# Kernel tuning notes

Measured on AMD Instinct MI355X. Metric: run time of the kernel, lower is better.

Reference implementation:

```python
import jax, jax.numpy as jnp
import numpy as np

V, NSEG, MAXLEN, D, H = 32000, 2, 512, 768, 12
HS = D // H  # head_size = 64
B, T, NMASK = 16, 512, 20
LN_EPS = 1e-5


def setup_inputs() -> dict:
    key = jax.random.key(0)
    ks = jax.random.split(key, 16)
    s = 0.02
    return {
        "sequence": jax.random.randint(ks[0], (B, T), 0, V),
        "segment": jax.random.randint(ks[1], (B, T), 0, NSEG),
        "attn_mask": jax.random.randint(ks[2], (B, T), 0, 2).astype(jnp.int32),
        "masked_pos": jax.random.randint(ks[3], (B, NMASK), 0, T),
        "tok_emb": jax.random.normal(ks[4], (V, D), jnp.float32) * s,
        "seg_emb": jax.random.normal(ks[5], (NSEG, D), jnp.float32) * s,
        "pos_emb": jax.random.normal(ks[6], (MAXLEN, D), jnp.float32) * s,
        "ln_g": jnp.ones((D,), jnp.float32),
        "ln_b": jnp.zeros((D,), jnp.float32),
        "Wq": jax.random.normal(ks[7], (H, D, HS), jnp.float32) * s,
        "Wk": jax.random.normal(ks[8], (H, D, HS), jnp.float32) * s,
        "Wv": jax.random.normal(ks[9], (H, D, HS), jnp.float32) * s,
        "W_lm": jax.random.normal(ks[10], (D, V), jnp.float32) * s,
        "b_lm": jnp.zeros((V,), jnp.float32),
        "W_cls": jax.random.normal(ks[11], (D, 2), jnp.float32) * s,
        "b_cls": jnp.zeros((2,), jnp.float32),
    }


def reference(sequence, segment, attn_mask, masked_pos,
              tok_emb, seg_emb, pos_emb, ln_g, ln_b,
              Wq, Wk, Wv, W_lm, b_lm, W_cls, b_cls):
    Tlen = sequence.shape[1]
    # --- BERTEmbedding (dropout = identity in eval) ---
    emb = tok_emb[sequence] + seg_emb[segment] + pos_emb[jnp.arange(Tlen)][None]  # [B,T,D]
    mu = jnp.mean(emb, axis=-1, keepdims=True)
    var = jnp.mean(jnp.square(emb - mu), axis=-1, keepdims=True)
    x = (emb - mu) * jax.lax.rsqrt(var + LN_EPS) * ln_g + ln_b  # [B,T,D]

    # --- Multi-head attention (heads batched instead of Python loop) ---
    q = jnp.einsum('btd,hds->bhts', x, Wq)
    k = jnp.einsum('btd,hds->bhts', x, Wk)
    v = jnp.einsum('btd,hds->bhts', x, Wv)
    wei = jnp.einsum('bhts,bhus->bhtu', q, k) * (HS ** -0.5)  # [B,H,T,T]
    # original: wei.masked_fill(attn_mask[:, :, None] == 0, -1e-11) -> masks over query dim
    wei = jnp.where(attn_mask[:, None, :, None] == 0, jnp.float32(-1e-11), wei)
    wei = jax.nn.softmax(wei, axis=-1)
    out = jnp.einsum('bhtu,bhus->bhts', wei, v)  # [B,H,T,HS]
    x = out.transpose(0, 2, 1, 3).reshape(out.shape[0], Tlen, H * HS)  # cat heads -> [B,T,D]

    # --- Output heads ---
    x_masked = jnp.take_along_axis(x, masked_pos[:, :, None], axis=1)  # [B,NMASK,D]
    logits_lm = x_masked @ W_lm + b_lm          # [B,NMASK,V]
    logits_clsf = x[:, 0, :] @ W_cls + b_cls    # [B,2]
    return (logits_lm, logits_clsf)
```

## Files before the change

### kernel.cpp

```cpp
#include <hip/hip_runtime.h>
#include <hip/hip_bf16.h>

#define V_     32000
#define NSEG_  2
#define MAXLEN_ 512
#define D_     768
#define H_     12
#define HS_    64
#define B_     16
#define T_     512
#define NMASK_ 20
#define LN_EPS_ 1e-5f

typedef __hip_bfloat16 bf16;
typedef unsigned short ushortT;
typedef __attribute__((ext_vector_type(8))) short short8;
typedef __attribute__((ext_vector_type(4))) float f32x4;
typedef __attribute__((ext_vector_type(4))) unsigned int u32x4;

__device__ __forceinline__ ushortT f2bu(float f) {
    bf16 h = __float2bfloat16(f);
    return *reinterpret_cast<ushortT*>(&h);
}

__global__ void k_embed_ln(const int* __restrict__ seq, const int* __restrict__ seg,
                           const float* __restrict__ tok, const float* __restrict__ sege,
                           const float* __restrict__ pos, const float* __restrict__ g,
                           const float* __restrict__ bb, ushortT* __restrict__ xb) {
    int row = blockIdx.x;
    int t = row % T_;
    int tid = threadIdx.x;
    __shared__ float sbuf[D_];
    __shared__ float wsum[4], wsq[4];

    int sidx = seq[row];
    int gidx = seg[row];

    float lsum = 0.f, lsq = 0.f;
    for (int j = tid; j < D_; j += 256) {
        float e = tok[(size_t)sidx * D_ + j] + sege[(size_t)gidx * D_ + j] + pos[(size_t)t * D_ + j];
        sbuf[j] = e;
        lsum += e;
        lsq  += e * e;
    }
    #pragma unroll
    for (int o = 32; o > 0; o >>= 1) {
        lsum += __shfl_down(lsum, o);
        lsq  += __shfl_down(lsq, o);
    }
    if ((tid & 63) == 0) { wsum[tid >> 6] = lsum; wsq[tid >> 6] = lsq; }
    __syncthreads();
    float s  = wsum[0] + wsum[1] + wsum[2] + wsum[3];
    float sq = wsq[0] + wsq[1] + wsq[2] + wsq[3];
    float mean = s * (1.0f / D_);
    float var  = sq * (1.0f / D_) - mean * mean;
    float rstd = rsqrtf(var + LN_EPS_);
    for (int j = tid; j < D_; j += 256) {
        xb[(size_t)row * D_ + j] = f2bu((sbuf[j] - mean) * rstd * g[j] + bb[j]);
    }
}

__global__ void k_prep_wqkv(const float* __restrict__ Wq, const float* __restrict__ Wk,
                            const float* __restrict__ Wv, ushortT* __restrict__ Wt) {
    int blk = blockIdx.x;
    int which = blk / H_, h = blk % H_;
    int kc = blockIdx.y * 64;
    const float* W = (which == 0) ? Wq : (which == 1) ? Wk : Wv;
    __shared__ float tile[64][65];
    int tid = threadIdx.x, c = tid & 63, rgrp = tid >> 6;
    for (int kk = rgrp; kk < 64; kk += 4)
        tile[kk][c] = W[((size_t)h * D_ + kc + kk) * HS_ + c];
    __syncthreads();
    for (int ss = rgrp; ss < 64; ss += 4)
        Wt[((size_t)which * D_ + h * HS_ + ss) * D_ + kc + c] = f2bu(tile[c][ss]);
}

__global__ void k_transpose_lm(const float* __restrict__ W, ushortT* __restrict__ Wt) {
    __shared__ float tile[64][65];
    int v0 = blockIdx.x * 64, d0 = blockIdx.y * 64;
    int tid = threadIdx.x, c = tid & 63;
    for (int rr = tid >> 6; rr < 64; rr += 4)
        tile[rr][c] = W[(size_t)(d0 + rr) * V_ + v0 + c];
    __syncthreads();
    for (int rr = tid >> 6; rr < 64; rr += 4)
        Wt[(size_t)(v0 + rr) * D_ + d0 + c] = f2bu(tile[c][rr]);
}

__global__ void k_gather_xm(const float* __restrict__ x2, const int* __restrict__ masked_pos,
                            ushortT* __restrict__ xm) {
    int r = blockIdx.x;
    int tid = threadIdx.x;
    if (r < B_ * NMASK_) {
        int b = r / NMASK_, m = r % NMASK_;
        int t = masked_pos[b * NMASK_ + m];
        for (int d = tid; d < D_; d += 256)
            xm[(size_t)r * D_ + d] = f2bu(x2[((size_t)b * T_ + t) * D_ + d]);
    } else {
        for (int d = tid; d < D_; d += 256)
            xm[(size_t)r * D_ + d] = 0;
    }
}

__device__ __forceinline__ void stage_tile(const ushortT* __restrict__ A,
                                           const ushortT* __restrict__ Bt,
                                           int m0, int n0, int k0,
                                           ushortT* As, ushortT* Bs,
                                           int w, int lane) {
    #pragma unroll
    for (int i = 0; i < 2; ++i) {
        int slot = w * 64 + lane + i * 256;
        int row = slot >> 2, col = (slot & 3) * 8;
        __builtin_amdgcn_global_load_lds(
            (const __attribute__((address_space(1))) void*)(A + (size_t)(m0 + row) * D_ + k0 + col),
            (__attribute__((address_space(3))) void*)(As + (w * 64 + i * 256) * 8),
            16, 0, 0);
        __builtin_amdgcn_global_load_lds(
            (const __attribute__((address_space(1))) void*)(Bt + (size_t)(n0 + row) * D_ + k0 + col),
            (__attribute__((address_space(3))) void*)(Bs + (w * 64 + i * 256) * 8),
            16, 0, 0);
    }
}

__device__ __forceinline__ void gemm128_2ph(const ushortT* __restrict__ A,
                                            const ushortT* __restrict__ Bt,
                                            int m0, int n0,
                                            ushortT* lds,
                                            f32x4 acc[4][4]) {
    const int NT = D_ / 32;
    int tid = threadIdx.x;
    int lane = tid & 63, w = tid >> 6;
    int wr = (w >> 1) * 64, wc = (w & 1) * 64;
    int l16 = lane & 15, lk = lane >> 4;

    #pragma unroll
    for (int i = 0; i < 4; ++i)
        #pragma unroll
        for (int j = 0; j < 4; ++j)
            acc[i][j] = (f32x4){0.f, 0.f, 0.f, 0.f};

    stage_tile(A, Bt, m0, n0, 0, lds, lds + 4096, w, lane);
    asm volatile("s_waitcnt vmcnt(0)" ::: "memory");
    __builtin_amdgcn_s_barrier();

    for (int t = 0; t < NT; ++t) {
        int cur = (t & 1) * 8192;
        int nxt = 8192 - cur;
        if (t + 1 < NT)
            stage_tile(A, Bt, m0, n0, (t + 1) * 32, lds + nxt, lds + nxt + 4096, w, lane);

        const ushortT* Asc = lds + cur;
        const ushortT* Bsc = lds + cur + 4096;
        short8 a[4], bfr[4];
        #pragma unroll
        for (int i = 0; i < 4; ++i) {
            a[i]   = *(const short8*)(Asc + (wr + i * 16 + l16) * 32 + lk * 8);
            bfr[i] = *(const short8*)(Bsc + (wc + i * 16 + l16) * 32 + lk * 8);
        }
        #pragma unroll
        for (int i = 0; i < 4; ++i)
            #pragma unroll
            for (int j = 0; j < 4; ++j)
                acc[i][j] = __builtin_amdgcn_mfma_f32_16x16x32_bf16(a[i], bfr[j], acc[i][j], 0, 0, 0);

        asm volatile("s_waitcnt vmcnt(0)" ::: "memory");
        __builtin_amdgcn_s_barrier();
    }
}

__global__ __launch_bounds__(256, 4)
void k_gemm_qkv(const ushortT* __restrict__ xb, const ushortT* __restrict__ WcatT,
                ushortT* __restrict__ qb, ushortT* __restrict__ kb,
                ushortT* __restrict__ vb) {
    __shared__ ushortT lds[16384];
    f32x4 acc[4][4];
    int lin = (blockIdx.x & 7) * 144 + (blockIdx.x >> 3);
    int n0 = (lin % 18) * 128, m0 = (lin / 18) * 128;
    gemm128_2ph(xb, WcatT, m0, n0, lds, acc);

    int lane = threadIdx.x & 63, w = threadIdx.x >> 6;
    int wr = (w >> 1) * 64, wc = (w & 1) * 64;
    int l16 = lane & 15, lk = lane >> 4;
    #pragma unroll
    for (int j = 0; j < 4; ++j) {
        int n = n0 + wc + j * 16 + l16;
        int which = n / D_;
        int rem = n - which * D_;
        int h = rem >> 6, s = rem & 63;
        ushortT* outp = (which == 0) ? qb : (which == 1) ? kb : vb;
        #pragma unroll
        for (int i = 0; i < 4; ++i) {
            #pragma unroll
            for (int r = 0; r < 4; ++r) {
                int m = m0 + wr + i * 16 + lk * 4 + r;
                int b = m >> 9, t = m & (T_ - 1);
                outp[((size_t)(b * H_ + h) * T_ + t) * HS_ + s] = f2bu(acc[i][j][r]);
            }
        }
    }
}

__global__ __launch_bounds__(256, 4)
void k_gemm_lm(const ushortT* __restrict__ xm, const ushortT* __restrict__ WlmT,
               const float* __restrict__ blm, float* __restrict__ out) {
    __shared__ ushortT lds[16384];
    f32x4 acc[4][4];
    int m0 = blockIdx.x * 128, n0 = blockIdx.y * 128;
    gemm128_2ph(xm, WlmT, m0, n0, lds, acc);

    int lane = threadIdx.x & 63, w = threadIdx.x >> 6;
    int wr = (w >> 1) * 64, wc = (w & 1) * 64;
    int l16 = lane & 15, lk = lane >> 4;
    #pragma unroll
    for (int j = 0; j < 4; ++j) {
        int n = n0 + wc + j * 16 + l16;
        float bias = blm[n];
        #pragma unroll
        for (int i = 0; i < 4; ++i) {
            #pragma unroll
            for (int r = 0; r < 4; ++r) {
                int m = m0 + wr + i * 16 + lk * 4 + r;
                if (m < B_ * NMASK_)
                    out[(size_t)m * V_ + n] = acc[i][j][r] + bias;
            }
        }
    }
}

__global__ __launch_bounds__(256, 4)
void k_attn_mfma(const ushortT* __restrict__ qb, const ushortT* __restrict__ kb,
                 const ushortT* __restrict__ vb, const int* __restrict__ attn_mask,
                 float* __restrict__ x2) {
    int lin = (blockIdx.x & 7) * 192 + (blockIdx.x >> 3);
    int qt = lin & 7, bh = lin >> 3;
    int b = bh / H_, h = bh % H_;
    int tid = threadIdx.x, lane = tid & 63, w = tid >> 6;
    int l16 = lane & 15, lk = lane >> 4;

    __shared__ ushortT QP[64][72];
    __shared__ ushortT Ks[64][72];
    __shared__ ushortT Vts[64][72];
    __shared__ float mskS[64];

    const ushortT* Qg = qb + ((size_t)bh * T_ + qt * 64) * HS_;
    #pragma unroll
    for (int i = 0; i < 2; ++i) {
        int slot = tid + i * 256;
        int r = slot >> 3, c8 = (slot & 7) * 8;
        *(u32x4*)(&QP[r][c8]) = *(const u32x4*)(Qg + (size_t)r * HS_ + c8);
    }
    if (tid < 64)
        mskS[tid] = attn_mask[b * T_ + qt * 64 + tid] ? 0.125f : 0.0f;
    __syncthreads();

    short8 aq[2];
    #pragma unroll
    for (int ks = 0; ks < 2; ++ks)
        aq[ks] = *(const short8*)(&QP[w * 16 + l16][ks * 32 + lk * 8]);
    float mrow[4];
    #pragma unroll
    for (int r = 0; r < 4; ++r)
        mrow[r] = mskS[w * 16 + lk * 4 + r];

    float lsum[4];
    f32x4 accO[4];
    #pragma unroll
    for (int r = 0; r < 4; ++r) lsum[r] = 0.f;
    #pragma unroll
    for (int j = 0; j < 4; ++j)
        accO[j] = (f32x4){0.f, 0.f, 0.f, 0.f};

    for (int kt = 0; kt < 8; ++kt) {
        __syncthreads();
        {
            int r = tid >> 2, c = (tid & 3) * 16;
            const ushortT* Kg = kb + ((size_t)bh * T_ + kt * 64 + r) * HS_ + c;
            *(u32x4*)(&Ks[r][c])     = *(const u32x4*)(Kg);
            *(u32x4*)(&Ks[r][c + 8]) = *(const u32x4*)(Kg + 8);
        }
        {
            int r = lane;
            int c = w * 16;
            const ushortT* Vg = vb + ((size_t)bh * T_ + kt * 64 + r) * HS_ + c;
            short8 v0 = *(const short8*)(Vg);
            short8 v1 = *(const short8*)(Vg + 8);
            #pragma unroll
            for (int e = 0; e < 8; ++e) Vts[c + e][r]     = (ushortT)v0[e];
            #pragma unroll
            for (int e = 0; e < 8; ++e) Vts[c + 8 + e][r] = (ushortT)v1[e];
        }
        __syncthreads();

        f32x4 accS[4];
        #pragma unroll
        for (int j = 0; j < 4; ++j)
            accS[j] = (f32x4){0.f, 0.f, 0.f, 0.f};
        #pragma unroll
        for (int ks = 0; ks < 2; ++ks) {
            short8 bk[4];
            #pragma unroll
            for (int j = 0; j < 4; ++j)
                bk[j] = *(const short8*)(&Ks[j * 16 + l16][ks * 32 + lk * 8]);
            #pragma unroll
            for (int j = 0; j < 4; ++j)
                accS[j] = __builtin_amdgcn_mfma_f32_16x16x32_bf16(aq[ks], bk[j], accS[j], 0, 0, 0);
        }

        #pragma unroll
        for (int r = 0; r < 4; ++r) {
            int rowl = lk * 4 + r;
            float m = mrow[r];
            float p0 = __expf(accS[0][r] * m);
            float p1 = __expf(accS[1][r] * m);
            float p2 = __expf(accS[2][r] * m);
            float p3 = __expf(accS[3][r] * m);
            lsum[r] += (p0 + p1) + (p2 + p3);
            QP[w * 16 + rowl][0 * 16 + l16] = f2bu(p0);
            QP[w * 16 + rowl][1 * 16 + l16] = f2bu(p1);
            QP[w * 16 + rowl][2 * 16 + l16] = f2bu(p2);
            QP[w * 16 + rowl][3 * 16 + l16] = f2bu(p3);
        }

        #pragma unroll
        for (int ks2 = 0; ks2 < 2; ++ks2) {
            short8 ap = *(const short8*)(&QP[w * 16 + l16][ks2 * 32 + lk * 8]);
            short8 bv[4];
            #pragma unroll
            for (int j = 0; j < 4; ++j)
                bv[j] = *(const short8*)(&Vts[j * 16 + l16][ks2 * 32 + lk * 8]);
            #pragma unroll
            for (int j = 0; j < 4; ++j)
                accO[j] = __builtin_amdgcn_mfma_f32_16x16x32_bf16(ap, bv[j], accO[j], 0, 0, 0);
        }
    }

    #pragma unroll
    for (int r = 0; r < 4; ++r) {
        float s = lsum[r];
        #pragma unroll
        for (int off = 1; off < 16; off <<= 1)
            s += __shfl_xor(s, off);
        float inv = 1.0f / s;
        int t = qt * 64 + w * 16 + lk * 4 + r;
        float* outp = x2 + ((size_t)b * T_ + t) * D_ + h * HS_;
        #pragma unroll
        for (int j = 0; j < 4; ++j)
            outp[j * 16 + l16] = accO[j][r] * inv;
    }
}

__global__ void k_cls(const float* __restrict__ x2, const float* __restrict__ Wc,
                      const float* __restrict__ bc, float* __restrict__ out) {
    int b = blockIdx.x;
    int tid = threadIdx.x;
    __shared__ float red0[4], red1[4];
    float a0 = 0.f, a1 = 0.f;
    const float* xr = x2 + (size_t)b * T_ * D_;
    for (int d = tid; d < D_; d += 256) {
        float x = xr[d];
        a0 += x * Wc[d * 2];
        a1 += x * Wc[d * 2 + 1];
    }
    #pragma unroll
    for (int o = 32; o > 0; o >>= 1) {
        a0 += __shfl_down(a0, o);
        a1 += __shfl_down(a1, o);
    }
    if ((tid & 63) == 0) { red0[tid >> 6] = a0; red1[tid >> 6] = a1; }
    __syncthreads();
    if (tid == 0)
        out[b * 2]     = red0[0] + red0[1] + red0[2] + red0[3] + bc[0];
    if (tid == 1)
        out[b * 2 + 1] = red1[0] + red1[1] + red1[2] + red1[3] + bc[1];
}

extern "C" void kernel_launch(void* const* d_in, const int* in_sizes, int n_in,
                              void* d_out, int out_size, void* d_ws, size_t ws_size,
                              hipStream_t stream) {
    const int* seq        = (const int*)d_in[0];
    const int* seg        = (const int*)d_in[1];
    const int* attn_mask  = (const int*)d_in[2];
    const int* masked_pos = (const int*)d_in[3];
    const float* tok  = (const float*)d_in[4];
    const float* sege = (const float*)d_in[5];
    const float* pos  = (const float*)d_in[6];
    const float* ln_g = (const float*)d_in[7];
    const float* ln_b = (const float*)d_in[8];
    const float* Wq   = (const float*)d_in[9];
    const float* Wk   = (const float*)d_in[10];
    const float* Wv   = (const float*)d_in[11];
    const float* Wlm  = (const float*)d_in[12];
    const float* blm  = (const float*)d_in[13];
    const float* Wc   = (const float*)d_in[14];
    const float* bc   = (const float*)d_in[15];

    float* out_lm  = (float*)d_out;
    float* out_cls = out_lm + (size_t)B_ * NMASK_ * V_;

    const size_t XSZ = (size_t)B_ * T_ * D_;
    float* ws = (float*)d_ws;
    float*   x2   = ws;
    ushortT* base = (ushortT*)(ws + XSZ);
    ushortT* xb    = base;
    ushortT* qb    = base + XSZ;
    ushortT* kb    = base + 2 * XSZ;
    ushortT* vb    = base + 3 * XSZ;
    ushortT* WcatT = base + 4 * XSZ;
    ushortT* WlmT  = base;
    ushortT* xm    = base + (size_t)V_ * D_;

    k_embed_ln<<<B_ * T_, 256, 0, stream>>>(seq, seg, tok, sege, pos, ln_g, ln_b, xb);
    k_prep_wqkv<<<dim3(3 * H_, 12), 256, 0, stream>>>(Wq, Wk, Wv, WcatT);
    k_gemm_qkv<<<1152, 256, 0, stream>>>(xb, WcatT, qb, kb, vb);
    k_attn_mfma<<<192 * 8, 256, 0, stream>>>(qb, kb, vb, attn_mask, x2);
    k_transpose_lm<<<dim3(V_ / 64, D_ / 64), 256, 0, stream>>>(Wlm, WlmT);
    k_gather_xm<<<384, 256, 0, stream>>>(x2, masked_pos, xm);
    k_gemm_lm<<<dim3(3, 250), 256, 0, stream>>>(xm, WlmT, blm, out_lm);
    k_cls<<<B_, 256, 0, stream>>>(x2, Wc, bc, out_cls);
}
```

Baseline: 171.2 us.

## Vectorize embed-LN, swizzle GEMM LDS tiles, stage QKV epilogue through LDS

The embedding+LayerNorm kernel now runs 192 threads, each loading and storing one float4/bf16x4, so the shared-memory buffer and strided loops go away. The GEMM staging applies an XOR swizzle on the 16-byte column chunk, both where tiles are written into LDS and where they are read back, to cut LDS bank conflicts. The QKV GEMM epilogue first writes its tile to padded LDS and then emits 16-byte coalesced stores into the per-head q/k/v layout, replacing scattered 2-byte stores. The larger LDS footprint (128x136) may reduce occupancy.

```diff
diff --git a/kernel.cpp b/kernel.cpp
--- a/kernel.cpp
+++ b/kernel.cpp
@@ -17,6 +17,7 @@
 typedef __attribute__((ext_vector_type(8))) short short8;
 typedef __attribute__((ext_vector_type(4))) float f32x4;
 typedef __attribute__((ext_vector_type(4))) unsigned int u32x4;
+typedef __attribute__((ext_vector_type(4))) unsigned short u16x4;
 
 __device__ __forceinline__ ushortT f2bu(float f) {
     bf16 h = __float2bfloat16(f);
@@ -28,36 +29,42 @@
                            const float* __restrict__ pos, const float* __restrict__ g,
                            const float* __restrict__ bb, ushortT* __restrict__ xb) {
     int row = blockIdx.x;
-    int t = row % T_;
+    int t = row & (T_ - 1);
     int tid = threadIdx.x;
-    __shared__ float sbuf[D_];
-    __shared__ float wsum[4], wsq[4];
+    __shared__ float wsum[3], wsq[3];
 
     int sidx = seq[row];
     int gidx = seg[row];
 
-    float lsum = 0.f, lsq = 0.f;
-    for (int j = tid; j < D_; j += 256) {
-        float e = tok[(size_t)sidx * D_ + j] + sege[(size_t)gidx * D_ + j] + pos[(size_t)t * D_ + j];
-        sbuf[j] = e;
-        lsum += e;
-        lsq  += e * e;
-    }
+    f32x4 e = *(const f32x4*)(tok  + (size_t)sidx * D_ + tid * 4);
+    f32x4 e2 = *(const f32x4*)(sege + (size_t)gidx * D_ + tid * 4);
+    f32x4 e3 = *(const f32x4*)(pos  + (size_t)t    * D_ + tid * 4);
+    e = e + e2 + e3;
+
+    float ls = e.x + e.y + e.z + e.w;
+    float lq = e.x * e.x + e.y * e.y + e.z * e.z + e.w * e.w;
     #pragma unroll
     for (int o = 32; o > 0; o >>= 1) {
-        lsum += __shfl_down(lsum, o);
-        lsq  += __shfl_down(lsq, o);
-    }
-    if ((tid & 63) == 0) { wsum[tid >> 6] = lsum; wsq[tid >> 6] = lsq; }
-    __syncthreads();
-    float s  = wsum[0] + wsum[1] + wsum[2] + wsum[3];
-    float sq = wsq[0] + wsq[1] + wsq[2] + wsq[3];
+        ls += __shfl_down(ls, o);
+        lq += __shfl_down(lq, o);
+    }
+    if ((tid & 63) == 0) { wsum[tid >> 6] = ls; wsq[tid >> 6] = lq; }
+    __syncthreads();
+    float s  = wsum[0] + wsum[1] + wsum[2];
+    float sq = wsq[0] + wsq[1] + wsq[2];
     float mean = s * (1.0f / D_);
     float var  = sq * (1.0f / D_) - mean * mean;
     float rstd = rsqrtf(var + LN_EPS_);
-    for (int j = tid; j < D_; j += 256) {
-        xb[(size_t)row * D_ + j] = f2bu((sbuf[j] - mean) * rstd * g[j] + bb[j]);
-    }
+
+    f32x4 g4 = *(const f32x4*)(g  + tid * 4);
+    f32x4 b4 = *(const f32x4*)(bb + tid * 4);
+    f32x4 x4;
+    x4.x = (e.x - mean) * rstd * g4.x + b4.x;
+    x4.y = (e.y - mean) * rstd * g4.y + b4.y;
+    x4.z = (e.z - mean) * rstd * g4.z + b4.z;
+    x4.w = (e.w - mean) * rstd * g4.w + b4.w;
+    u16x4 ov = {f2bu(x4.x), f2bu(x4.y), f2bu(x4.z), f2bu(x4.w)};
+    *(u16x4*)(xb + (size_t)row * D_ + tid * 4) = ov;
 }
 
 __global__ void k_prep_wqkv(const float* __restrict__ Wq, const float* __restrict__ Wk,
@@ -109,13 +116,14 @@
     #pragma unroll
     for (int i = 0; i < 2; ++i) {
         int slot = w * 64 + lane + i * 256;
-        int row = slot >> 2, col = (slot & 3) * 8;
+        int row = slot >> 2;
+        int cs = ((slot & 3) ^ (row & 3)) * 8;
         __builtin_amdgcn_global_load_lds(
-            (const __attribute__((address_space(1))) void*)(A + (size_t)(m0 + row) * D_ + k0 + col),
+            (const __attribute__((address_space(1))) void*)(A + (size_t)(m0 + row) * D_ + k0 + cs),
             (__attribute__((address_space(3))) void*)(As + (w * 64 + i * 256) * 8),
             16, 0, 0);
         __builtin_amdgcn_global_load_lds(
-            (const __attribute__((address_space(1))) void*)(Bt + (size_t)(n0 + row) * D_ + k0 + col),
+            (const __attribute__((address_space(1))) void*)(Bt + (size_t)(n0 + row) * D_ + k0 + cs),
             (__attribute__((address_space(3))) void*)(Bs + (w * 64 + i * 256) * 8),
             16, 0, 0);
     }
@@ -131,6 +139,7 @@
     int lane = tid & 63, w = tid >> 6;
     int wr = (w >> 1) * 64, wc = (w & 1) * 64;
     int l16 = lane & 15, lk = lane >> 4;
+    int sw = (lk ^ (l16 & 3)) * 8;
 
     #pragma unroll
     for (int i = 0; i < 4; ++i)
@@ -153,8 +162,8 @@
         short8 a[4], bfr[4];
         #pragma unroll
         for (int i = 0; i < 4; ++i) {
-            a[i]   = *(const short8*)(Asc + (wr + i * 16 + l16) * 32 + lk * 8);
-            bfr[i] = *(const short8*)(Bsc + (wc + i * 16 + l16) * 32 + lk * 8);
+            a[i]   = *(const short8*)(Asc + (wr + i * 16 + l16) * 32 + sw);
+            bfr[i] = *(const short8*)(Bsc + (wc + i * 16 + l16) * 32 + sw);
         }
         #pragma unroll
         for (int i = 0; i < 4; ++i)
@@ -171,31 +180,45 @@
 void k_gemm_qkv(const ushortT* __restrict__ xb, const ushortT* __restrict__ WcatT,
                 ushortT* __restrict__ qb, ushortT* __restrict__ kb,
                 ushortT* __restrict__ vb) {
-    __shared__ ushortT lds[16384];
+    __shared__ ushortT lds[128 * 136];
     f32x4 acc[4][4];
     int lin = (blockIdx.x & 7) * 144 + (blockIdx.x >> 3);
     int n0 = (lin % 18) * 128, m0 = (lin / 18) * 128;
     gemm128_2ph(xb, WcatT, m0, n0, lds, acc);
 
-    int lane = threadIdx.x & 63, w = threadIdx.x >> 6;
+    int tid = threadIdx.x;
+    int lane = tid & 63, w = tid >> 6;
     int wr = (w >> 1) * 64, wc = (w & 1) * 64;
     int l16 = lane & 15, lk = lane >> 4;
+
     #pragma unroll
     for (int j = 0; j < 4; ++j) {
-        int n = n0 + wc + j * 16 + l16;
-        int which = n / D_;
-        int rem = n - which * D_;
-        int h = rem >> 6, s = rem & 63;
-        ushortT* outp = (which == 0) ? qb : (which == 1) ? kb : vb;
+        int n = wc + j * 16 + l16;
         #pragma unroll
         for (int i = 0; i < 4; ++i) {
             #pragma unroll
             for (int r = 0; r < 4; ++r) {
-                int m = m0 + wr + i * 16 + lk * 4 + r;
-                int b = m >> 9, t = m & (T_ - 1);
-                outp[((size_t)(b * H_ + h) * T_ + t) * HS_ + s] = f2bu(acc[i][j][r]);
+                int m = wr + i * 16 + lk * 4 + r;
+                lds[m * 136 + n] = f2bu(acc[i][j][r]);
             }
         }
+    }
+    __syncthreads();
+
+    int which = n0 / D_;
+    int nrem0 = n0 - which * D_;
+    ushortT* outp = (which == 0) ? qb : (which == 1) ? kb : vb;
+    int b = m0 >> 9;
+    int t0 = m0 & (T_ - 1);
+    #pragma unroll
+    for (int p = 0; p < 8; ++p) {
+        int chunk = p * 256 + tid;
+        int row = chunk >> 4;
+        int nc = (chunk & 15) * 8;
+        int h = (nrem0 >> 6) + (nc >> 6);
+        int s0 = nc & 63;
+        u32x4 v = *(const u32x4*)(&lds[row * 136 + nc]);
+        *(u32x4*)(outp + ((size_t)(b * H_ + h) * T_ + (t0 + row)) * HS_ + s0) = v;
     }
 }
 
@@ -408,7 +431,7 @@
     ushortT* WlmT  = base;
     ushortT* xm    = base + (size_t)V_ * D_;
 
-    k_embed_ln<<<B_ * T_, 256, 0, stream>>>(seq, seg, tok, sege, pos, ln_g, ln_b, xb);
+    k_embed_ln<<<B_ * T_, 192, 0, stream>>>(seq, seg, tok, sege, pos, ln_g, ln_b, xb);
     k_prep_wqkv<<<dim3(3 * H_, 12), 256, 0, stream>>>(Wq, Wk, Wv, WcatT);
     k_gemm_qkv<<<1152, 256, 0, stream>>>(xb, WcatT, qb, kb, vb);
     k_attn_mfma<<<192 * 8, 256, 0, stream>>>(qb, kb, vb, attn_mask, x2);
```

Measured after the change: 163.4 us. 4.6% less time.
